# Optimization experiments

Hardware: AMD Instinct MI355X
Metric: run time of the kernel (lower is better)

## Reference

```python
import jax, jax.numpy as jnp
import numpy as np

B = 8
T, H, W = 8, 56, 56
C = 128
NH = 4
HD = C // NH
WS = (2, 7, 7)
SS = (1, 3, 3)
N = WS[0] * WS[1] * WS[2]  # 98 tokens per window
HID = 4 * C
SCALE = HD ** -0.5
RPB_SIZE = (2 * WS[0] - 1) * (2 * WS[1] - 1) * (2 * WS[2] - 1)  # 507
EPS = 1e-5


def _rel_index():
    # [N, N] int index into relative position bias table
    coords = np.stack(np.meshgrid(np.arange(WS[0]), np.arange(WS[1]), np.arange(WS[2]), indexing='ij'))
    cf = coords.reshape(3, -1)
    rel = (cf[:, :, None] - cf[:, None, :]).transpose(1, 2, 0)
    rel[:, :, 0] += WS[0] - 1
    rel[:, :, 1] += WS[1] - 1
    rel[:, :, 2] += WS[2] - 1
    rel[:, :, 0] *= (2 * WS[1] - 1) * (2 * WS[2] - 1)
    rel[:, :, 1] *= 2 * WS[2] - 1
    return rel.sum(-1)


def _np_window_partition_mask(img):
    # img: [1,T,H,W,1] -> [nW, N]
    m = img.reshape(1, T // WS[0], WS[0], H // WS[1], WS[1], W // WS[2], WS[2], 1)
    m = m.transpose(0, 1, 3, 5, 2, 4, 6, 7).reshape(-1, N)
    return m


def _attn_mask():
    # standard shifted-window mask: [nW, N, N] with 0 / -100
    img = np.zeros((1, T, H, W, 1), np.float32)
    cnt = 0
    slices = lambda w, s: (slice(0, -w), slice(-w, -s), slice(-s, None))
    for t in slices(WS[0], SS[0]):
        for h in slices(WS[1], SS[1]):
            for w in slices(WS[2], SS[2]):
                img[:, t, h, w, :] = cnt
                cnt += 1
    mw = _np_window_partition_mask(img)
    am = mw[:, None, :] - mw[:, :, None]
    return np.where(am != 0, np.float32(-100.0), np.float32(0.0))


REL_IDX = jnp.asarray(_rel_index())          # [N, N]
ATTN_MASK = jnp.asarray(_attn_mask())        # [nW, N, N]


def window_partition(x):
    # x: [B,T,H,W,C] -> [B*nW, N, C]
    x = x.reshape(B, T // WS[0], WS[0], H // WS[1], WS[1], W // WS[2], WS[2], C)
    return x.transpose(0, 1, 3, 5, 2, 4, 6, 7).reshape(-1, N, C)


def window_reverse(w):
    # w: [B*nW, N, C] -> [B,T,H,W,C]
    x = w.reshape(B, T // WS[0], H // WS[1], W // WS[2], WS[0], WS[1], WS[2], C)
    return x.transpose(0, 1, 4, 2, 5, 3, 6, 7).reshape(B, T, H, W, C)


def layernorm(x, g, b):
    mu = x.mean(-1, keepdims=True)
    var = ((x - mu) ** 2).mean(-1, keepdims=True)
    return (x - mu) * jax.lax.rsqrt(var + EPS) * g + b


def setup_inputs() -> dict:
    key = jax.random.key(0)
    ks = jax.random.split(key, 8)
    p = lambda k, shp: jax.random.normal(k, shp, jnp.float32) * 0.02
    return {
        'x': jax.random.normal(ks[0], (B, T * H * W, C), jnp.float32),
        'norm1_g': jnp.ones((C,), jnp.float32), 'norm1_b': jnp.zeros((C,), jnp.float32),
        'qkv_w': p(ks[1], (C, 3 * C)), 'qkv_b': jnp.zeros((3 * C,), jnp.float32),
        'proj_w': p(ks[2], (C, C)), 'proj_b': jnp.zeros((C,), jnp.float32),
        'rpb_table': p(ks[3], (RPB_SIZE, NH)),
        'norm2_g': jnp.ones((C,), jnp.float32), 'norm2_b': jnp.zeros((C,), jnp.float32),
        'fc1_w': p(ks[4], (C, HID)), 'fc1_b': jnp.zeros((HID,), jnp.float32),
        'fc2_w': p(ks[5], (HID, C)), 'fc2_b': jnp.zeros((C,), jnp.float32),
    }


def reference(x, norm1_g, norm1_b, qkv_w, qkv_b, proj_w, proj_b, rpb_table,
              norm2_g, norm2_b, fc1_w, fc1_b, fc2_w, fc2_b):
    shortcut = x
    h = layernorm(x, norm1_g, norm1_b).reshape(B, T, H, W, C)
    # cyclic shift
    h = jnp.roll(h, (-SS[0], -SS[1], -SS[2]), axis=(1, 2, 3))
    xw = window_partition(h)                                   # [B_, N, C]
    B_ = xw.shape[0]
    qkv = (xw @ qkv_w + qkv_b).reshape(B_, N, 3, NH, HD)
    qkv = qkv.transpose(2, 0, 3, 1, 4)                         # [3, B_, NH, N, HD]
    q, k, v = qkv[0] * SCALE, qkv[1], qkv[2]
    attn = jnp.einsum('bhnd,bhmd->bhnm', q, k)                 # [B_, NH, N, N]
    bias = rpb_table[REL_IDX.reshape(-1)].reshape(N, N, NH).transpose(2, 0, 1)
    attn = attn + bias[None]
    nW = ATTN_MASK.shape[0]
    attn = attn.reshape(B_ // nW, nW, NH, N, N) + ATTN_MASK[None, :, None]
    attn = jax.nn.softmax(attn.reshape(B_, NH, N, N), axis=-1)
    out = jnp.einsum('bhnm,bhmd->bhnd', attn, v)               # [B_, NH, N, HD]
    out = out.transpose(0, 2, 1, 3).reshape(B_, N, C)
    out = out @ proj_w + proj_b
    h = window_reverse(out)
    h = jnp.roll(h, SS, axis=(1, 2, 3)).reshape(B, T * H * W, C)
    x = shortcut + h
    y = layernorm(x, norm2_g, norm2_b)
    y = jax.nn.gelu(y @ fc1_w + fc1_b, approximate=False) @ fc2_w + fc2_b
    return x + y
```

## Files before the change

### kernel.cpp

```cpp
#include <hip/hip_runtime.h>
#include <hip/hip_bf16.h>
#include <cmath>

using bf16 = __hip_bfloat16;
typedef __attribute__((ext_vector_type(8))) short short8;
typedef __attribute__((ext_vector_type(4))) short short4v;
typedef __attribute__((ext_vector_type(4))) float float4f;

#define THW 25088
#define SCALE_QK 0.17677669529663687f

static __device__ __forceinline__ float4f mfma16(short8 a, short8 b, float4f c) {
  return __builtin_amdgcn_mfma_f32_16x16x32_bf16(a, b, c, 0, 0, 0);
}
static __device__ __forceinline__ short8 load8(const bf16* p) {
  return *reinterpret_cast<const short8*>(p);
}
static __device__ __forceinline__ short8 load8u(const unsigned short* p) {
  return *reinterpret_cast<const short8*>(p);
}
static __device__ __forceinline__ bf16 f2b(float v) { return __float2bfloat16(v); }
static __device__ __forceinline__ unsigned short f2bits(float v) {
  bf16 h = __float2bfloat16(v);
  unsigned short u; __builtin_memcpy(&u, &h, 2); return u;
}
static __device__ __forceinline__ float bits2f(unsigned short u) {
  unsigned int w = ((unsigned int)u) << 16;
  float f; __builtin_memcpy(&f, &w, 4); return f;
}
static __device__ __forceinline__ float gelu_f(float v) {
  float y = 0.7978845608028654f * (v + 0.044715f * v * v * v);
  float e = __expf(-2.f * fabsf(y));
  float t = 1.f - 2.f * e / (1.f + e);
  return 0.5f * v * (1.f + copysignf(t, y));
}

__global__ __launch_bounds__(256) void transpose_all(
    const float* __restrict__ qkv_w, const float* __restrict__ proj_w,
    const float* __restrict__ fc1_w, const float* __restrict__ fc2_w,
    const float* __restrict__ rpb,
    bf16* __restrict__ bq, bf16* __restrict__ bp,
    bf16* __restrict__ b1, bf16* __restrict__ b2,
    unsigned short* __restrict__ tbl) {
  int idx = blockIdx.x * 256 + threadIdx.x;
  if (idx < 49152) {
    int k = idx / 384, n = idx - k * 384;
    float v = qkv_w[idx];
    if (n < 128) v *= SCALE_QK;
    bq[(size_t)n * 128 + k] = f2b(v);
  } else if (idx < 65536) {
    int i = idx - 49152;
    int k = i / 128, n = i - k * 128;
    bp[(size_t)n * 128 + k] = f2b(proj_w[i]);
  } else if (idx < 131072) {
    int i = idx - 65536;
    int k = i / 512, n = i - k * 512;
    b1[(size_t)n * 128 + k] = f2b(fc1_w[i]);
  } else if (idx < 196608) {
    int i = idx - 131072;
    int k = i / 128, n = i - k * 128;
    b2[(size_t)n * 512 + k] = f2b(fc2_w[i]);
  } else {
    int i2 = idx - 196608;
    int col = i2 % 120; int rest = i2 / 120;
    int row = rest % 112; rest /= 112;
    int head = rest & 3; int cat = rest >> 2;
    int i = row > 97 ? 97 : row;
    int j = col > 97 ? 97 : col;
    int ti = i / 49, ri = i - ti * 49, hi = ri / 7, wi = ri - hi * 7;
    int tj = j / 49, rj = j - tj * 49, hj = rj / 7, wj = rj - hj * 7;
    int tbit = (cat >> 2) & 1, hbit = (cat >> 1) & 1, wbit = cat & 1;
    int ilab = (tbit ? 1 + ti : 0) * 9 + (hbit ? 1 + (hi >= 4) : 0) * 3 +
               (wbit ? 1 + (wi >= 4) : 0);
    int jlab = (tbit ? 1 + tj : 0) * 9 + (hbit ? 1 + (hj >= 4) : 0) * 3 +
               (wbit ? 1 + (wj >= 4) : 0);
    int idxr = (ti - tj + 1) * 169 + (hi - hj + 6) * 13 + (wi - wj + 6);
    float v = rpb[idxr * 4 + head];
    if (ilab != jlab) v -= 100.f;
    if (col >= 98) v = -30000.f;
    tbl[i2] = f2bits(v);
  }
}

__global__ __launch_bounds__(1024) void win_k(const float* __restrict__ x,
    const float* __restrict__ n1g, const float* __restrict__ n1b,
    const bf16* __restrict__ bt_qkv, const float* __restrict__ qkv_b,
    const bf16* __restrict__ bt_proj, const float* __restrict__ proj_b,
    const float* __restrict__ n2g, const float* __restrict__ n2b,
    const bf16* __restrict__ bt_fc1, const float* __restrict__ fc1b,
    const bf16* __restrict__ bt_fc2, const float* __restrict__ fc2b,
    const unsigned short* __restrict__ tbl, float* __restrict__ out) {
  __shared__ __align__(16) unsigned short qk[112][264];
  __shared__ __align__(16) unsigned short vt[128][136];
  __shared__ __align__(16) unsigned short pool[16 * 16 * 136];
  auto xn   = reinterpret_cast<unsigned short(*)[136]>(pool);
  auto Pl   = reinterpret_cast<unsigned short(*)[16][136]>(pool);
  auto xmid = reinterpret_cast<float(*)[132]>(pool);

  const int lane = threadIdx.x & 63, wave = threadIdx.x >> 6;
  const int l15 = lane & 15, lq = lane >> 4;
  const int wg = blockIdx.x;
  const int batch = wg >> 8, widx = wg & 255;
  const int tw = widx >> 6, hw = (widx >> 3) & 7, ww = widx & 7;
  const int cat = ((tw == 3) ? 4 : 0) + ((hw == 7) ? 2 : 0) + ((ww == 7) ? 1 : 0);

  for (int i = threadIdx.x; i < 128 * 16; i += 1024) {
    vt[i >> 4][112 + (i & 15)] = 0;
  }

  {
    float2 gp = reinterpret_cast<const float2*>(n1g)[lane];
    float2 bp = reinterpret_cast<const float2*>(n1b)[lane];
    float2 vals[7];
    #pragma unroll
    for (int i = 0; i < 7; i++) {
      int lrow = wave * 7 + i;
      int n = lrow > 97 ? 97 : lrow;
      int ti = n / 49, rr = n - ti * 49, hi = rr / 7, wi = rr - hi * 7;
      int t = (tw * 2 + ti + 1) & 7;
      int h = hw * 7 + hi + 3; if (h >= 56) h -= 56;
      int w = ww * 7 + wi + 3; if (w >= 56) w -= 56;
      unsigned int tok = (unsigned int)batch * THW + (t * 56 + h) * 56 + w;
      if (lane == 0) *reinterpret_cast<unsigned int*>(&vt[lrow][128]) = tok;
      vals[i] = reinterpret_cast<const float2*>(x + (size_t)tok * 128)[lane];
    }
    #pragma unroll
    for (int i = 0; i < 7; i++) {
      int lrow = wave * 7 + i;
      float2 v = vals[i];
      float s = v.x + v.y, ss = v.x * v.x + v.y * v.y;
      #pragma unroll
      for (int m = 1; m < 64; m <<= 1) { s += __shfl_xor(s, m); ss += __shfl_xor(ss, m); }
      float mu = s * (1.f / 128.f);
      float var = ss * (1.f / 128.f) - mu * mu;
      float rs = rsqrtf(var + 1e-5f);
      float o0 = (v.x - mu) * rs * gp.x + bp.x;
      float o1 = (v.y - mu) * rs * gp.y + bp.y;
      *reinterpret_cast<unsigned int*>(&xn[lrow][lane * 2]) =
          (unsigned int)f2bits(o0) | ((unsigned int)f2bits(o1) << 16);
    }
  }
  __syncthreads();

  for (int task = wave; task < 48; task += 16) {
    const int ct = task >> 1, half = task & 1;
    const int rt0 = half ? 4 : 0, rt1 = half ? 7 : 4;
    short8 wf[4];
    #pragma unroll
    for (int q = 0; q < 4; q++)
      wf[q] = load8(bt_qkv + (size_t)(ct * 16 + l15) * 128 + q * 32 + lq * 8);
    if (ct < 16) {
      float4f bs = *reinterpret_cast<const float4f*>(qkv_b + ct * 16 + lq * 4);
      if (ct < 8) bs *= SCALE_QK;
      const int colb = (ct < 8 ? ct * 16 : 128 + (ct - 8) * 16) + lq * 4;
      #pragma unroll
      for (int i = 0; i < 4; i++) {
        int rt = rt0 + i;
        if (rt < rt1) {
          float4f acc = (float4f){0.f, 0.f, 0.f, 0.f};
          #pragma unroll
          for (int q = 0; q < 4; q++)
            acc = mfma16(wf[q], load8u(&xn[rt * 16 + l15][q * 32 + lq * 8]), acc);
          short4v pk;
          #pragma unroll
          for (int r = 0; r < 4; r++) pk[r] = (short)f2bits(acc[r] + bs[r]);
          *reinterpret_cast<short4v*>(&qk[rt * 16 + l15][colb]) = pk;
        }
      }
    } else {
      const float bsv = qkv_b[256 + (ct - 16) * 16 + l15];
      #pragma unroll
      for (int i = 0; i < 4; i++) {
        int rt = rt0 + i;
        if (rt < rt1) {
          float4f acc = (float4f){0.f, 0.f, 0.f, 0.f};
          #pragma unroll
          for (int q = 0; q < 4; q++)
            acc = mfma16(load8u(&xn[rt * 16 + l15][q * 32 + lq * 8]), wf[q], acc);
          short4v pk;
          #pragma unroll
          for (int r = 0; r < 4; r++) pk[r] = (short)f2bits(acc[r] + bsv);
          *reinterpret_cast<short4v*>(&vt[(ct - 16) * 16 + l15][rt * 16 + lq * 4]) = pk;
        }
      }
    }
  }
  __syncthreads();

  for (int task = wave; task < 28; task += 16) {
    const int head = task & 3, rb = task >> 2;
    const int q0 = rb * 16;
    const unsigned short* tb =
        tbl + ((size_t)(cat * 4 + head) * 112 + (q0 + l15)) * 120;

    short8 aq = load8u(&qk[q0 + l15][head * 32 + lq * 8]);
    float pv[7][4];
    float sum = 0.f;
    #pragma unroll
    for (int t = 0; t < 7; t++) {
      short8 kb = load8u(&qk[t * 16 + l15][128 + head * 32 + lq * 8]);
      float4f s = mfma16(kb, aq, (float4f){0.f, 0.f, 0.f, 0.f});
      short4v bv = *reinterpret_cast<const short4v*>(tb + t * 16 + lq * 4);
      #pragma unroll
      for (int r = 0; r < 4; r++) {
        float p = __expf(s[r] + bits2f((unsigned short)bv[r]));
        pv[t][r] = p; sum += p;
      }
    }
    sum += __shfl_xor(sum, 16);
    sum += __shfl_xor(sum, 32);
    float inv = 1.f / sum;
    #pragma unroll
    for (int t = 0; t < 7; t++) {
      short4v pk;
      #pragma unroll
      for (int r = 0; r < 4; r++) pk[r] = (short)f2bits(pv[t][r] * inv);
      *reinterpret_cast<short4v*>(&Pl[wave][l15][t * 16 + lq * 4]) = pk;
    }
    *reinterpret_cast<short4v*>(&Pl[wave][l15][112 + lq * 4]) = (short4v){0, 0, 0, 0};

    float4f o0 = (float4f){0.f, 0.f, 0.f, 0.f};
    float4f o1 = (float4f){0.f, 0.f, 0.f, 0.f};
    #pragma unroll
    for (int ks = 0; ks < 4; ks++) {
      short8 pf = load8u(&Pl[wave][l15][ks * 32 + lq * 8]);
      o0 = mfma16(load8u(&vt[head * 32 + l15][ks * 32 + lq * 8]), pf, o0);
      o1 = mfma16(load8u(&vt[head * 32 + 16 + l15][ks * 32 + lq * 8]), pf, o1);
    }
    short4v k0, k1;
    #pragma unroll
    for (int r = 0; r < 4; r++) {
      k0[r] = (short)f2bits(o0[r]);
      k1[r] = (short)f2bits(o1[r]);
    }
    *reinterpret_cast<short4v*>(&qk[q0 + l15][head * 32 + lq * 4]) = k0;
    *reinterpret_cast<short4v*>(&qk[q0 + l15][head * 32 + 16 + lq * 4]) = k1;
  }
  __syncthreads();

  const int ct4 = wave & 7, half4 = wave >> 3;
  const int rt0 = half4 ? 4 : 0, rt1 = half4 ? 7 : 4;
  const int cb = ct4 * 16 + lq * 4;
  float4f xmr[4];
  {
    float4f pb = *reinterpret_cast<const float4f*>(proj_b + cb);
    short8 wf[4];
    #pragma unroll
    for (int q = 0; q < 4; q++)
      wf[q] = load8(bt_proj + (size_t)(ct4 * 16 + l15) * 128 + q * 32 + lq * 8);
    #pragma unroll
    for (int i = 0; i < 4; i++) {
      int rt = rt0 + i;
      if (rt < rt1) {
        float4f acc = (float4f){0.f, 0.f, 0.f, 0.f};
        #pragma unroll
        for (int q = 0; q < 4; q++)
          acc = mfma16(wf[q], load8u(&qk[rt * 16 + l15][q * 32 + lq * 8]), acc);
        int row = rt * 16 + l15;
        if (row < 98) {
          unsigned int tok = *reinterpret_cast<const unsigned int*>(&vt[row][128]);
          float4f xv = *reinterpret_cast<const float4f*>(x + (size_t)tok * 128 + cb);
          float4f res = xv + acc + pb;
          xmr[i] = res;
          *reinterpret_cast<float4f*>(&xmid[row][cb]) = res;
        }
      }
    }
  }
  __syncthreads();

  {
    float2 gp = reinterpret_cast<const float2*>(n2g)[lane];
    float2 bp = reinterpret_cast<const float2*>(n2b)[lane];
    #pragma unroll
    for (int i = 0; i < 7; i++) {
      int lrow = wave * 7 + i;
      int n = lrow > 97 ? 97 : lrow;
      float2 v = *reinterpret_cast<const float2*>(&xmid[n][lane * 2]);
      float s = v.x + v.y, ss = v.x * v.x + v.y * v.y;
      #pragma unroll
      for (int m = 1; m < 64; m <<= 1) { s += __shfl_xor(s, m); ss += __shfl_xor(ss, m); }
      float mu = s * (1.f / 128.f);
      float var = ss * (1.f / 128.f) - mu * mu;
      float rs = rsqrtf(var + 1e-5f);
      float o0 = (v.x - mu) * rs * gp.x + bp.x;
      float o1 = (v.y - mu) * rs * gp.y + bp.y;
      *reinterpret_cast<unsigned int*>(&vt[lrow][lane * 2]) =
          (unsigned int)f2bits(o0) | ((unsigned int)f2bits(o1) << 16);
    }
  }
  __syncthreads();

  float4f acc2[4];
  #pragma unroll
  for (int i = 0; i < 4; i++) acc2[i] = (float4f){0.f, 0.f, 0.f, 0.f};
  const int hc = wave * 16 + lq * 4;

  float4f a1[7];
  {
    short8 w1[4];
    #pragma unroll
    for (int q = 0; q < 4; q++)
      w1[q] = load8(bt_fc1 + (size_t)(wave * 16 + l15) * 128 + q * 32 + lq * 8);
    float4f b1v = *reinterpret_cast<const float4f*>(fc1b + hc);
    #pragma unroll
    for (int rt = 0; rt < 7; rt++) {
      float4f acc = (float4f){0.f, 0.f, 0.f, 0.f};
      #pragma unroll
      for (int q = 0; q < 4; q++)
        acc = mfma16(w1[q], load8u(&vt[rt * 16 + l15][q * 32 + lq * 8]), acc);
      #pragma unroll
      for (int r = 0; r < 4; r++) acc[r] = gelu_f(acc[r] + b1v[r]);
      a1[rt] = acc;
    }
  }
  #pragma unroll
  for (int rt = 0; rt < 7; rt++) {
    short4v pk;
    #pragma unroll
    for (int r = 0; r < 4; r++) pk[r] = (short)f2bits(a1[rt][r]);
    *reinterpret_cast<short4v*>(&qk[rt * 16 + l15][hc]) = pk;
  }
  __syncthreads();

  {
    short8 w1[4];
    #pragma unroll
    for (int q = 0; q < 4; q++)
      w1[q] = load8(bt_fc1 + (size_t)(256 + wave * 16 + l15) * 128 + q * 32 + lq * 8);
    float4f b1v = *reinterpret_cast<const float4f*>(fc1b + 256 + hc);
    short8 w2[4];
    #pragma unroll
    for (int q = 0; q < 4; q++)
      w2[q] = load8(bt_fc2 + (size_t)(ct4 * 16 + l15) * 512 + q * 32 + lq * 8);
    #pragma unroll
    for (int rt = 0; rt < 7; rt++) {
      float4f acc = (float4f){0.f, 0.f, 0.f, 0.f};
      #pragma unroll
      for (int q = 0; q < 4; q++)
        acc = mfma16(w1[q], load8u(&vt[rt * 16 + l15][q * 32 + lq * 8]), acc);
      #pragma unroll
      for (int r = 0; r < 4; r++) acc[r] = gelu_f(acc[r] + b1v[r]);
      a1[rt] = acc;
    }
    #pragma unroll
    for (int i = 0; i < 4; i++) {
      int rt = rt0 + i;
      if (rt < rt1) {
        #pragma unroll
        for (int q = 0; q < 4; q++)
          acc2[i] = mfma16(w2[q], load8u(&qk[rt * 16 + l15][q * 32 + lq * 8]), acc2[i]);
      }
    }
    short8 w2b[4];
    #pragma unroll
    for (int q = 0; q < 4; q++)
      w2b[q] = load8(bt_fc2 + (size_t)(ct4 * 16 + l15) * 512 + 128 + q * 32 + lq * 8);
    #pragma unroll
    for (int i = 0; i < 4; i++) {
      int rt = rt0 + i;
      if (rt < rt1) {
        #pragma unroll
        for (int q = 0; q < 4; q++)
          acc2[i] = mfma16(w2b[q], load8u(&qk[rt * 16 + l15][128 + q * 32 + lq * 8]), acc2[i]);
      }
    }
  }
  __syncthreads();
  #pragma unroll
  for (int rt = 0; rt < 7; rt++) {
    short4v pk;
    #pragma unroll
    for (int r = 0; r < 4; r++) pk[r] = (short)f2bits(a1[rt][r]);
    *reinterpret_cast<short4v*>(&qk[rt * 16 + l15][hc]) = pk;
  }
  __syncthreads();
  {
    short8 w2[4];
    #pragma unroll
    for (int q = 0; q < 4; q++)
      w2[q] = load8(bt_fc2 + (size_t)(ct4 * 16 + l15) * 512 + 256 + q * 32 + lq * 8);
    #pragma unroll
    for (int i = 0; i < 4; i++) {
      int rt = rt0 + i;
      if (rt < rt1) {
        #pragma unroll
        for (int q = 0; q < 4; q++)
          acc2[i] = mfma16(w2[q], load8u(&qk[rt * 16 + l15][q * 32 + lq * 8]), acc2[i]);
      }
    }
    short8 w2b[4];
    #pragma unroll
    for (int q = 0; q < 4; q++)
      w2b[q] = load8(bt_fc2 + (size_t)(ct4 * 16 + l15) * 512 + 384 + q * 32 + lq * 8);
    #pragma unroll
    for (int i = 0; i < 4; i++) {
      int rt = rt0 + i;
      if (rt < rt1) {
        #pragma unroll
        for (int q = 0; q < 4; q++)
          acc2[i] = mfma16(w2b[q], load8u(&qk[rt * 16 + l15][128 + q * 32 + lq * 8]), acc2[i]);
      }
    }
  }

  {
    float4f b2v = *reinterpret_cast<const float4f*>(fc2b + cb);
    #pragma unroll
    for (int i = 0; i < 4; i++) {
      int rt = rt0 + i;
      if (rt < rt1) {
        int row = rt * 16 + l15;
        if (row < 98) {
          unsigned int tok = *reinterpret_cast<const unsigned int*>(&vt[row][128]);
          *reinterpret_cast<float4f*>(out + (size_t)tok * 128 + cb) = xmr[i] + acc2[i] + b2v;
        }
      }
    }
  }
}

extern "C" void kernel_launch(void* const* d_in, const int* in_sizes, int n_in,
                              void* d_out, int out_size, void* d_ws, size_t ws_size,
                              hipStream_t stream) {
  (void)in_sizes; (void)n_in; (void)out_size; (void)ws_size;
  const float* x      = (const float*)d_in[0];
  const float* n1g    = (const float*)d_in[1];
  const float* n1b    = (const float*)d_in[2];
  const float* qkv_w  = (const float*)d_in[3];
  const float* qkv_b  = (const float*)d_in[4];
  const float* proj_w = (const float*)d_in[5];
  const float* proj_b = (const float*)d_in[6];
  const float* rpb    = (const float*)d_in[7];
  const float* n2g    = (const float*)d_in[8];
  const float* n2b    = (const float*)d_in[9];
  const float* fc1_w  = (const float*)d_in[10];
  const float* fc1_b  = (const float*)d_in[11];
  const float* fc2_w  = (const float*)d_in[12];
  const float* fc2_b  = (const float*)d_in[13];
  float* out = (float*)d_out;

  char* ws = (char*)d_ws;
  bf16* bt_qkv  = (bf16*)(ws + 0);
  bf16* bt_proj = (bf16*)(ws + 98304);
  bf16* bt_fc1  = (bf16*)(ws + 131072);
  bf16* bt_fc2  = (bf16*)(ws + 262144);
  unsigned short* tbl = (unsigned short*)(ws + 393216);

  transpose_all<<<2448, 256, 0, stream>>>(qkv_w, proj_w, fc1_w, fc2_w, rpb,
                                          bt_qkv, bt_proj, bt_fc1, bt_fc2, tbl);

  win_k<<<2048, 1024, 0, stream>>>(x, n1g, n1b, bt_qkv, qkv_b, bt_proj, proj_b,
                                   n2g, n2b, bt_fc1, fc1_b, bt_fc2, fc2_b,
                                   tbl, out);
}
```

Baseline: 522.3 us.

## Prefetch weights and bias tables before barriers and remap LayerNorm lanes

```diff
diff --git a/kernel.cpp b/kernel.cpp
--- a/kernel.cpp
+++ b/kernel.cpp
@@ -103,96 +103,130 @@
   const int batch = wg >> 8, widx = wg & 255;
   const int tw = widx >> 6, hw = (widx >> 3) & 7, ww = widx & 7;
   const int cat = ((tw == 3) ? 4 : 0) + ((hw == 7) ? 2 : 0) + ((ww == 7) ? 1 : 0);
+  const int cg = l15 * 8;
 
   for (int i = threadIdx.x; i < 128 * 16; i += 1024) {
     vt[i >> 4][112 + (i & 15)] = 0;
   }
 
   {
-    float2 gp = reinterpret_cast<const float2*>(n1g)[lane];
-    float2 bp = reinterpret_cast<const float2*>(n1b)[lane];
-    float2 vals[7];
-    #pragma unroll
-    for (int i = 0; i < 7; i++) {
-      int lrow = wave * 7 + i;
-      int n = lrow > 97 ? 97 : lrow;
+    float4f g0 = *reinterpret_cast<const float4f*>(n1g + cg);
+    float4f g1 = *reinterpret_cast<const float4f*>(n1g + cg + 4);
+    float4f b0 = *reinterpret_cast<const float4f*>(n1b + cg);
+    float4f b1 = *reinterpret_cast<const float4f*>(n1b + cg + 4);
+    #pragma unroll
+    for (int p = 0; p < 2; p++) {
+      int slot = p * 4 + lq;
+      int lrow = wave * 7 + slot;
+      bool valid = slot < 7;
+      int n = (!valid || lrow > 97) ? 97 : lrow;
       int ti = n / 49, rr = n - ti * 49, hi = rr / 7, wi = rr - hi * 7;
       int t = (tw * 2 + ti + 1) & 7;
       int h = hw * 7 + hi + 3; if (h >= 56) h -= 56;
       int w = ww * 7 + wi + 3; if (w >= 56) w -= 56;
       unsigned int tok = (unsigned int)batch * THW + (t * 56 + h) * 56 + w;
-      if (lane == 0) *reinterpret_cast<unsigned int*>(&vt[lrow][128]) = tok;
-      vals[i] = reinterpret_cast<const float2*>(x + (size_t)tok * 128)[lane];
-    }
-    #pragma unroll
-    for (int i = 0; i < 7; i++) {
-      int lrow = wave * 7 + i;
-      float2 v = vals[i];
-      float s = v.x + v.y, ss = v.x * v.x + v.y * v.y;
-      #pragma unroll
-      for (int m = 1; m < 64; m <<= 1) { s += __shfl_xor(s, m); ss += __shfl_xor(ss, m); }
+      if (valid && l15 == 0) *reinterpret_cast<unsigned int*>(&vt[lrow][128]) = tok;
+      const float* xp = x + (size_t)tok * 128 + cg;
+      float4f a = *reinterpret_cast<const float4f*>(xp);
+      float4f b = *reinterpret_cast<const float4f*>(xp + 4);
+      float s = (a[0] + a[1]) + (a[2] + a[3]) + (b[0] + b[1]) + (b[2] + b[3]);
+      float ss = a[0]*a[0] + a[1]*a[1] + a[2]*a[2] + a[3]*a[3]
+               + b[0]*b[0] + b[1]*b[1] + b[2]*b[2] + b[3]*b[3];
+      s += __shfl_xor(s, 1);  ss += __shfl_xor(ss, 1);
+      s += __shfl_xor(s, 2);  ss += __shfl_xor(ss, 2);
+      s += __shfl_xor(s, 4);  ss += __shfl_xor(ss, 4);
+      s += __shfl_xor(s, 8);  ss += __shfl_xor(ss, 8);
       float mu = s * (1.f / 128.f);
       float var = ss * (1.f / 128.f) - mu * mu;
       float rs = rsqrtf(var + 1e-5f);
-      float o0 = (v.x - mu) * rs * gp.x + bp.x;
-      float o1 = (v.y - mu) * rs * gp.y + bp.y;
-      *reinterpret_cast<unsigned int*>(&xn[lrow][lane * 2]) =
-          (unsigned int)f2bits(o0) | ((unsigned int)f2bits(o1) << 16);
-    }
-  }
-  __syncthreads();
-
-  for (int task = wave; task < 48; task += 16) {
-    const int ct = task >> 1, half = task & 1;
-    const int rt0 = half ? 4 : 0, rt1 = half ? 7 : 4;
-    short8 wf[4];
-    #pragma unroll
-    for (int q = 0; q < 4; q++)
-      wf[q] = load8(bt_qkv + (size_t)(ct * 16 + l15) * 128 + q * 32 + lq * 8);
-    if (ct < 16) {
-      float4f bs = *reinterpret_cast<const float4f*>(qkv_b + ct * 16 + lq * 4);
-      if (ct < 8) bs *= SCALE_QK;
-      const int colb = (ct < 8 ? ct * 16 : 128 + (ct - 8) * 16) + lq * 4;
-      #pragma unroll
-      for (int i = 0; i < 4; i++) {
-        int rt = rt0 + i;
-        if (rt < rt1) {
-          float4f acc = (float4f){0.f, 0.f, 0.f, 0.f};
-          #pragma unroll
-          for (int q = 0; q < 4; q++)
-            acc = mfma16(wf[q], load8u(&xn[rt * 16 + l15][q * 32 + lq * 8]), acc);
-          short4v pk;
-          #pragma unroll
-          for (int r = 0; r < 4; r++) pk[r] = (short)f2bits(acc[r] + bs[r]);
-          *reinterpret_cast<short4v*>(&qk[rt * 16 + l15][colb]) = pk;
-        }
-      }
-    } else {
-      const float bsv = qkv_b[256 + (ct - 16) * 16 + l15];
-      #pragma unroll
-      for (int i = 0; i < 4; i++) {
-        int rt = rt0 + i;
-        if (rt < rt1) {
-          float4f acc = (float4f){0.f, 0.f, 0.f, 0.f};
-          #pragma unroll
-          for (int q = 0; q < 4; q++)
-            acc = mfma16(load8u(&xn[rt * 16 + l15][q * 32 + lq * 8]), wf[q], acc);
-          short4v pk;
-          #pragma unroll
-          for (int r = 0; r < 4; r++) pk[r] = (short)f2bits(acc[r] + bsv);
-          *reinterpret_cast<short4v*>(&vt[(ct - 16) * 16 + l15][rt * 16 + lq * 4]) = pk;
-        }
-      }
-    }
-  }
-  __syncthreads();
-
-  for (int task = wave; task < 28; task += 16) {
-    const int head = task & 3, rb = task >> 2;
-    const int q0 = rb * 16;
+      short8 pk;
+      pk[0] = (short)f2bits((a[0] - mu) * rs * g0[0] + b0[0]);
+      pk[1] = (short)f2bits((a[1] - mu) * rs * g0[1] + b0[1]);
+      pk[2] = (short)f2bits((a[2] - mu) * rs * g0[2] + b0[2]);
+      pk[3] = (short)f2bits((a[3] - mu) * rs * g0[3] + b0[3]);
+      pk[4] = (short)f2bits((b[0] - mu) * rs * g1[0] + b1[0]);
+      pk[5] = (short)f2bits((b[1] - mu) * rs * g1[1] + b1[1]);
+      pk[6] = (short)f2bits((b[2] - mu) * rs * g1[2] + b1[2]);
+      pk[7] = (short)f2bits((b[3] - mu) * rs * g1[3] + b1[3]);
+      if (valid) *reinterpret_cast<short8*>(&xn[lrow][cg]) = pk;
+    }
+  }
+
+  const int c0 = wave >> 1, halfq = wave & 1;
+  const int rtq0 = halfq ? 4 : 0, rtq1 = halfq ? 7 : 4;
+  short8 wfQ[4], wfK[4];
+  #pragma unroll
+  for (int q = 0; q < 4; q++) {
+    wfQ[q] = load8(bt_qkv + (size_t)(c0 * 16 + l15) * 128 + q * 32 + lq * 8);
+    wfK[q] = load8(bt_qkv + (size_t)((c0 + 8) * 16 + l15) * 128 + q * 32 + lq * 8);
+  }
+  __syncthreads();
+
+  {
+    float4f bsq = *reinterpret_cast<const float4f*>(qkv_b + c0 * 16 + lq * 4);
+    bsq *= SCALE_QK;
+    #pragma unroll
+    for (int i = 0; i < 4; i++) {
+      int rt = rtq0 + i;
+      if (rt < rtq1) {
+        float4f acc = (float4f){0.f, 0.f, 0.f, 0.f};
+        #pragma unroll
+        for (int q = 0; q < 4; q++)
+          acc = mfma16(wfQ[q], load8u(&xn[rt * 16 + l15][q * 32 + lq * 8]), acc);
+        short4v pk;
+        #pragma unroll
+        for (int r = 0; r < 4; r++) pk[r] = (short)f2bits(acc[r] + bsq[r]);
+        *reinterpret_cast<short4v*>(&qk[rt * 16 + l15][c0 * 16 + lq * 4]) = pk;
+      }
+    }
+    float4f bsk = *reinterpret_cast<const float4f*>(qkv_b + 128 + c0 * 16 + lq * 4);
+    #pragma unroll
+    for (int i = 0; i < 4; i++) {
+      int rt = rtq0 + i;
+      if (rt < rtq1) {
+        float4f acc = (float4f){0.f, 0.f, 0.f, 0.f};
+        #pragma unroll
+        for (int q = 0; q < 4; q++)
+          acc = mfma16(wfK[q], load8u(&xn[rt * 16 + l15][q * 32 + lq * 8]), acc);
+        short4v pk;
+        #pragma unroll
+        for (int r = 0; r < 4; r++) pk[r] = (short)f2bits(acc[r] + bsk[r]);
+        *reinterpret_cast<short4v*>(&qk[rt * 16 + l15][128 + c0 * 16 + lq * 4]) = pk;
+      }
+    }
+    short8 wfV[4];
+    #pragma unroll
+    for (int q = 0; q < 4; q++)
+      wfV[q] = load8(bt_qkv + (size_t)((c0 + 16) * 16 + l15) * 128 + q * 32 + lq * 8);
+    const float bsv = qkv_b[256 + c0 * 16 + l15];
+    #pragma unroll
+    for (int i = 0; i < 4; i++) {
+      int rt = rtq0 + i;
+      if (rt < rtq1) {
+        float4f acc = (float4f){0.f, 0.f, 0.f, 0.f};
+        #pragma unroll
+        for (int q = 0; q < 4; q++)
+          acc = mfma16(load8u(&xn[rt * 16 + l15][q * 32 + lq * 8]), wfV[q], acc);
+        short4v pk;
+        #pragma unroll
+        for (int r = 0; r < 4; r++) pk[r] = (short)f2bits(acc[r] + bsv);
+        *reinterpret_cast<short4v*>(&vt[c0 * 16 + l15][rt * 16 + lq * 4]) = pk;
+      }
+    }
+  }
+
+  const int head0 = wave & 3, rb0 = wave >> 2;
+  short4v tb0[7];
+  {
     const unsigned short* tb =
-        tbl + ((size_t)(cat * 4 + head) * 112 + (q0 + l15)) * 120;
-
+        tbl + ((size_t)(cat * 4 + head0) * 112 + (rb0 * 16 + l15)) * 120;
+    #pragma unroll
+    for (int t = 0; t < 7; t++)
+      tb0[t] = *reinterpret_cast<const short4v*>(tb + t * 16 + lq * 4);
+  }
+  __syncthreads();
+
+  auto attn_task = [&](int head, int q0, const short4v* tbv) {
     short8 aq = load8u(&qk[q0 + l15][head * 32 + lq * 8]);
     float pv[7][4];
     float sum = 0.f;
@@ -200,10 +234,9 @@
     for (int t = 0; t < 7; t++) {
       short8 kb = load8u(&qk[t * 16 + l15][128 + head * 32 + lq * 8]);
       float4f s = mfma16(kb, aq, (float4f){0.f, 0.f, 0.f, 0.f});
-      short4v bv = *reinterpret_cast<const short4v*>(tb + t * 16 + lq * 4);
       #pragma unroll
       for (int r = 0; r < 4; r++) {
-        float p = __expf(s[r] + bits2f((unsigned short)bv[r]));
+        float p = __expf(s[r] + bits2f((unsigned short)tbv[t][r]));
         pv[t][r] = p; sum += p;
       }
     }
@@ -235,112 +268,146 @@
     }
     *reinterpret_cast<short4v*>(&qk[q0 + l15][head * 32 + lq * 4]) = k0;
     *reinterpret_cast<short4v*>(&qk[q0 + l15][head * 32 + 16 + lq * 4]) = k1;
-  }
-  __syncthreads();
+  };
+
+  attn_task(head0, rb0 * 16, tb0);
+  if (rb0 < 3) {
+    short4v tb1[7];
+    const unsigned short* tb =
+        tbl + ((size_t)(cat * 4 + head0) * 112 + ((rb0 + 4) * 16 + l15)) * 120;
+    #pragma unroll
+    for (int t = 0; t < 7; t++)
+      tb1[t] = *reinterpret_cast<const short4v*>(tb + t * 16 + lq * 4);
+    attn_task(head0, (rb0 + 4) * 16, tb1);
+  }
 
   const int ct4 = wave & 7, half4 = wave >> 3;
   const int rt0 = half4 ? 4 : 0, rt1 = half4 ? 7 : 4;
   const int cb = ct4 * 16 + lq * 4;
+  short8 wfP[4];
+  #pragma unroll
+  for (int q = 0; q < 4; q++)
+    wfP[q] = load8(bt_proj + (size_t)(ct4 * 16 + l15) * 128 + q * 32 + lq * 8);
+  float4f pb = *reinterpret_cast<const float4f*>(proj_b + cb);
+  float4f xv[4];
+  #pragma unroll
+  for (int i = 0; i < 4; i++) {
+    int rt = rt0 + i;
+    if (rt < rt1) {
+      int row = rt * 16 + l15;
+      if (row < 98) {
+        unsigned int tok = *reinterpret_cast<const unsigned int*>(&vt[row][128]);
+        xv[i] = *reinterpret_cast<const float4f*>(x + (size_t)tok * 128 + cb);
+      }
+    }
+  }
+  __syncthreads();
+
   float4f xmr[4];
-  {
-    float4f pb = *reinterpret_cast<const float4f*>(proj_b + cb);
-    short8 wf[4];
-    #pragma unroll
-    for (int q = 0; q < 4; q++)
-      wf[q] = load8(bt_proj + (size_t)(ct4 * 16 + l15) * 128 + q * 32 + lq * 8);
-    #pragma unroll
-    for (int i = 0; i < 4; i++) {
-      int rt = rt0 + i;
-      if (rt < rt1) {
-        float4f acc = (float4f){0.f, 0.f, 0.f, 0.f};
-        #pragma unroll
-        for (int q = 0; q < 4; q++)
-          acc = mfma16(wf[q], load8u(&qk[rt * 16 + l15][q * 32 + lq * 8]), acc);
-        int row = rt * 16 + l15;
-        if (row < 98) {
-          unsigned int tok = *reinterpret_cast<const unsigned int*>(&vt[row][128]);
-          float4f xv = *reinterpret_cast<const float4f*>(x + (size_t)tok * 128 + cb);
-          float4f res = xv + acc + pb;
-          xmr[i] = res;
-          *reinterpret_cast<float4f*>(&xmid[row][cb]) = res;
-        }
-      }
-    }
-  }
-  __syncthreads();
-
-  {
-    float2 gp = reinterpret_cast<const float2*>(n2g)[lane];
-    float2 bp = reinterpret_cast<const float2*>(n2b)[lane];
-    #pragma unroll
-    for (int i = 0; i < 7; i++) {
-      int lrow = wave * 7 + i;
-      int n = lrow > 97 ? 97 : lrow;
-      float2 v = *reinterpret_cast<const float2*>(&xmid[n][lane * 2]);
-      float s = v.x + v.y, ss = v.x * v.x + v.y * v.y;
+  #pragma unroll
+  for (int i = 0; i < 4; i++) {
+    int rt = rt0 + i;
+    if (rt < rt1) {
+      float4f acc = (float4f){0.f, 0.f, 0.f, 0.f};
       #pragma unroll
-      for (int m = 1; m < 64; m <<= 1) { s += __shfl_xor(s, m); ss += __shfl_xor(ss, m); }
+      for (int q = 0; q < 4; q++)
+        acc = mfma16(wfP[q], load8u(&qk[rt * 16 + l15][q * 32 + lq * 8]), acc);
+      int row = rt * 16 + l15;
+      if (row < 98) {
+        float4f res = xv[i] + acc + pb;
+        xmr[i] = res;
+        *reinterpret_cast<float4f*>(&xmid[row][cb]) = res;
+      }
+    }
+  }
+  __syncthreads();
+
+  {
+    float4f g0 = *reinterpret_cast<const float4f*>(n2g + cg);
+    float4f g1 = *reinterpret_cast<const float4f*>(n2g + cg + 4);
+    float4f b0 = *reinterpret_cast<const float4f*>(n2b + cg);
+    float4f b1 = *reinterpret_cast<const float4f*>(n2b + cg + 4);
+    #pragma unroll
+    for (int p = 0; p < 2; p++) {
+      int slot = p * 4 + lq;
+      int lrow = wave * 7 + slot;
+      bool valid = slot < 7;
+      int n = (!valid || lrow > 97) ? 97 : lrow;
+      float4f a = *reinterpret_cast<const float4f*>(&xmid[n][cg]);
+      float4f b = *reinterpret_cast<const float4f*>(&xmid[n][cg + 4]);
+      float s = (a[0] + a[1]) + (a[2] + a[3]) + (b[0] + b[1]) + (b[2] + b[3]);
+      float ss = a[0]*a[0] + a[1]*a[1] + a[2]*a[2] + a[3]*a[3]
+               + b[0]*b[0] + b[1]*b[1] + b[2]*b[2] + b[3]*b[3];
+      s += __shfl_xor(s, 1);  ss += __shfl_xor(ss, 1);
+      s += __shfl_xor(s, 2);  ss += __shfl_xor(ss, 2);
+      s += __shfl_xor(s, 4);  ss += __shfl_xor(ss, 4);
+      s += __shfl_xor(s, 8);  ss += __shfl_xor(ss, 8);
       float mu = s * (1.f / 128.f);
       float var = ss * (1.f / 128.f) - mu * mu;
       float rs = rsqrtf(var + 1e-5f);
-      float o0 = (v.x - mu) * rs * gp.x + bp.x;
-      float o1 = (v.y - mu) * rs * gp.y + bp.y;
-      *reinterpret_cast<unsigned int*>(&vt[lrow][lane * 2]) =
-          (unsigned int)f2bits(o0) | ((unsigned int)f2bits(o1) << 16);
-    }
-  }
+      short8 pk;
+      pk[0] = (short)f2bits((a[0] - mu) * rs * g0[0] + b0[0]);
+      pk[1] = (short)f2bits((a[1] - mu) * rs * g0[1] + b0[1]);
+      pk[2] = (short)f2bits((a[2] - mu) * rs * g0[2] + b0[2]);
+      pk[3] = (short)f2bits((a[3] - mu) * rs * g0[3] + b0[3]);
+      pk[4] = (short)f2bits((b[0] - mu) * rs * g1[0] + b1[0]);
+      pk[5] = (short)f2bits((b[1] - mu) * rs * g1[1] + b1[1]);
+      pk[6] = (short)f2bits((b[2] - mu) * rs * g1[2] + b1[2]);
+      pk[7] = (short)f2bits((b[3] - mu) * rs * g1[3] + b1[3]);
+      if (valid) *reinterpret_cast<short8*>(&vt[lrow][cg]) = pk;
+    }
+  }
+
+  const int hc = wave * 16 + lq * 4;
+  short8 w1[4];
+  #pragma unroll
+  for (int q = 0; q < 4; q++)
+    w1[q] = load8(bt_fc1 + (size_t)(wave * 16 + l15) * 128 + q * 32 + lq * 8);
+  float4f b1v = *reinterpret_cast<const float4f*>(fc1b + hc);
   __syncthreads();
 
   float4f acc2[4];
   #pragma unroll
   for (int i = 0; i < 4; i++) acc2[i] = (float4f){0.f, 0.f, 0.f, 0.f};
-  const int hc = wave * 16 + lq * 4;
 
   float4f a1[7];
-  {
-    short8 w1[4];
-    #pragma unroll
-    for (int q = 0; q < 4; q++)
-      w1[q] = load8(bt_fc1 + (size_t)(wave * 16 + l15) * 128 + q * 32 + lq * 8);
-    float4f b1v = *reinterpret_cast<const float4f*>(fc1b + hc);
+  #pragma unroll
+  for (int rt = 0; rt < 7; rt++) {
+    float4f acc = (float4f){0.f, 0.f, 0.f, 0.f};
+    #pragma unroll
+    for (int q = 0; q < 4; q++)
+      acc = mfma16(w1[q], load8u(&vt[rt * 16 + l15][q * 32 + lq * 8]), acc);
+    #pragma unroll
+    for (int r = 0; r < 4; r++) acc[r] = gelu_f(acc[r] + b1v[r]);
+    a1[rt] = acc;
+  }
+  #pragma unroll
+  for (int rt = 0; rt < 7; rt++) {
+    short4v pk;
+    #pragma unroll
+    for (int r = 0; r < 4; r++) pk[r] = (short)f2bits(a1[rt][r]);
+    *reinterpret_cast<short4v*>(&qk[rt * 16 + l15][hc]) = pk;
+  }
+  __syncthreads();
+
+  {
+    short8 w1b[4];
+    #pragma unroll
+    for (int q = 0; q < 4; q++)
+      w1b[q] = load8(bt_fc1 + (size_t)(256 + wave * 16 + l15) * 128 + q * 32 + lq * 8);
+    float4f b1v2 = *reinterpret_cast<const float4f*>(fc1b + 256 + hc);
+    short8 w2[4];
+    #pragma unroll
+    for (int q = 0; q < 4; q++)
+      w2[q] = load8(bt_fc2 + (size_t)(ct4 * 16 + l15) * 512 + q * 32 + lq * 8);
     #pragma unroll
     for (int rt = 0; rt < 7; rt++) {
       float4f acc = (float4f){0.f, 0.f, 0.f, 0.f};
       #pragma unroll
       for (int q = 0; q < 4; q++)
-        acc = mfma16(w1[q], load8u(&vt[rt * 16 + l15][q * 32 + lq * 8]), acc);
+        acc = mfma16(w1b[q], load8u(&vt[rt * 16 + l15][q * 32 + lq * 8]), acc);
       #pragma unroll
-      for (int r = 0; r < 4; r++) acc[r] = gelu_f(acc[r] + b1v[r]);
-      a1[rt] = acc;
-    }
-  }
-  #pragma unroll
-  for (int rt = 0; rt < 7; rt++) {
-    short4v pk;
-    #pragma unroll
-    for (int r = 0; r < 4; r++) pk[r] = (short)f2bits(a1[rt][r]);
-    *reinterpret_cast<short4v*>(&qk[rt * 16 + l15][hc]) = pk;
-  }
-  __syncthreads();
-
-  {
-    short8 w1[4];
-    #pragma unroll
-    for (int q = 0; q < 4; q++)
-      w1[q] = load8(bt_fc1 + (size_t)(256 + wave * 16 + l15) * 128 + q * 32 + lq * 8);
-    float4f b1v = *reinterpret_cast<const float4f*>(fc1b + 256 + hc);
-    short8 w2[4];
-    #pragma unroll
-    for (int q = 0; q < 4; q++)
-      w2[q] = load8(bt_fc2 + (size_t)(ct4 * 16 + l15) * 512 + q * 32 + lq * 8);
-    #pragma unroll
-    for (int rt = 0; rt < 7; rt++) {
-      float4f acc = (float4f){0.f, 0.f, 0.f, 0.f};
-      #pragma unroll
-      for (int q = 0; q < 4; q++)
-        acc = mfma16(w1[q], load8u(&vt[rt * 16 + l15][q * 32 + lq * 8]), acc);
-      #pragma unroll
-      for (int r = 0; r < 4; r++) acc[r] = gelu_f(acc[r] + b1v[r]);
+      for (int r = 0; r < 4; r++) acc[r] = gelu_f(acc[r] + b1v2[r]);
       a1[rt] = acc;
     }
     #pragma unroll
```

Result: faster. 480.2 us (-8.1%).
